# Optimization experiments

Measured on AMD Instinct MI355X. Metric: run time of the kernel, lower is better.

The kernel has to match this reference:

```python
import jax, jax.numpy as jnp
import numpy as np

N_NODES = 50000
N_EDGES = 1600000
D = 128        # fea_dim == hidden_units == dim_z
L = 3          # num_layers


def _gin_params(key, scale=0.05):
    ks = jax.random.split(key, 7)
    return dict(
        W1=jax.random.normal(ks[0], (L, D, D), jnp.float32) * scale,
        b1=jnp.zeros((L, D), jnp.float32),
        W2=jax.random.normal(ks[1], (L, D, D), jnp.float32) * scale,
        b2=jnp.zeros((L, D), jnp.float32),
        eps=jnp.zeros((L,), jnp.float32),
        Wout=jax.random.normal(ks[2], (D, D), jnp.float32) * scale,
        bout=jnp.zeros((D,), jnp.float32),
    )


def setup_inputs() -> dict:
    key = jax.random.key(0)
    k_x, k_s, k_d, k_m, k_sd = jax.random.split(key, 5)
    inp = {
        'x': jax.random.normal(k_x, (N_NODES, D), jnp.float32),
        'edge_src': jax.random.randint(k_s, (N_EDGES,), 0, N_NODES, jnp.int32),
        'edge_dst': jax.random.randint(k_d, (N_EDGES,), 0, N_NODES, jnp.int32),
    }
    for pref, k in (('mean_', k_m), ('std_', k_sd)):
        for name, v in _gin_params(k).items():
            inp[pref + name] = v
    inp['ln_gamma'] = jnp.ones((D,), jnp.float32)
    inp['ln_beta'] = jnp.zeros((D,), jnp.float32)
    return inp


def _gin(x, src, dst, W1, b1, W2, b2, eps, Wout, bout):
    # Standard GIN: h = MLP((1+eps)*h + sum_{j->i} h_j), Sigmoid activation
    h = x
    n = x.shape[0]
    for l in range(L):
        agg = jax.ops.segment_sum(h[src], dst, num_segments=n)  # [N, D]
        h = (1.0 + eps[l]) * h + agg
        h = jax.nn.sigmoid(h @ W1[l] + b1[l]) @ W2[l] + b2[l]
    return h @ Wout + bout  # [N, dim_z]


def _layernorm(v, g, b, eps=1e-5):
    m = jnp.mean(v, axis=-1, keepdims=True)
    var = jnp.var(v, axis=-1, keepdims=True)
    return (v - m) * jax.lax.rsqrt(var + eps) * g + b


def reference(x, edge_src, edge_dst,
              mean_W1, mean_b1, mean_W2, mean_b2, mean_eps, mean_Wout, mean_bout,
              std_W1, std_b1, std_W2, std_b2, std_eps, std_Wout, std_bout,
              ln_gamma, ln_beta):
    mean_v = _layernorm(_gin(x, edge_src, edge_dst, mean_W1, mean_b1, mean_W2,
                             mean_b2, mean_eps, mean_Wout, mean_bout),
                        ln_gamma, ln_beta)
    # NOTE: source applies bn_mean to the std path too (faithful to bug)
    std_v = _layernorm(_gin(x, edge_src, edge_dst, std_W1, std_b1, std_W2,
                            std_b2, std_eps, std_Wout, std_bout),
                       ln_gamma, ln_beta)
    epsilon = jax.random.normal(jax.random.key(42), mean_v.shape, mean_v.dtype)
    samples = mean_v + epsilon * std_v
    return (samples, mean_v, std_v)
```

## Files before the change

kernel.cpp:

```cpp
#include <hip/hip_runtime.h>
#include <math.h>

#define NNODES 50000
#define NEDGES 1600000
#define DIM    128
#define NHID   (NNODES * DIM)
#define TPB    256
#define NTILES ((NNODES + 63) / 64)

#define NBINS  196
#define BINSZ  256
#define EPT    16
#define CHUNK  (TPB * EPT)
#define NCHUNKS ((NEDGES + CHUNK - 1) / CHUNK)
#define BINCAP 10240

typedef unsigned short bf16_t;
typedef __attribute__((ext_vector_type(8))) short short8;
typedef __attribute__((ext_vector_type(4))) float f32x4;

__device__ __forceinline__ float bf_lo(unsigned u) { return __uint_as_float(u << 16); }
__device__ __forceinline__ float bf_hi(unsigned u) { return __uint_as_float(u & 0xFFFF0000u); }
__device__ __forceinline__ bf16_t f2bf(float f) {
    unsigned u = __float_as_uint(f);
    u += 0x7FFFu + ((u >> 16) & 1u);
    return (bf16_t)(u >> 16);
}
__device__ __forceinline__ unsigned pack2bf(float a, float b) {
    return (unsigned)f2bf(a) | ((unsigned)f2bf(b) << 16);
}

union S8U { short8 v; uint4 u4; unsigned us[4]; };

__global__ __launch_bounds__(TPB) void bin_hist_kernel(
    const int* __restrict__ dst, int* __restrict__ gcnt)
{
    __shared__ int lcnt[NBINS];
    const int tid = threadIdx.x;
    for (int i = tid; i < NBINS; i += TPB) lcnt[i] = 0;
    __syncthreads();
    const int base = blockIdx.x * CHUNK;
    #pragma unroll
    for (int k = 0; k < EPT; ++k) {
        int e = base + k * TPB + tid;
        if (e < NEDGES) atomicAdd(&lcnt[dst[e] >> 8], 1);
    }
    __syncthreads();
    for (int i = tid; i < NBINS; i += TPB) {
        int c = lcnt[i];
        if (c) atomicAdd(&gcnt[i], c);
    }
}

__global__ __launch_bounds__(64) void bin_scan_kernel(
    const int* __restrict__ gcnt, int* __restrict__ start, int* __restrict__ bcur,
    int* __restrict__ off)
{
    const int lane = threadIdx.x;
    int c[4];
    int s = 0;
    #pragma unroll
    for (int k = 0; k < 4; ++k) {
        int b = 4 * lane + k;
        c[k] = (b < NBINS) ? gcnt[b] : 0;
        s += c[k];
    }
    int incl = s;
    #pragma unroll
    for (int d = 1; d < 64; d <<= 1) {
        int t = __shfl_up(incl, d);
        if (lane >= d) incl += t;
    }
    int excl = incl - s;
    #pragma unroll
    for (int k = 0; k < 4; ++k) {
        int b = 4 * lane + k;
        if (b < NBINS) { start[b] = excl; bcur[b] = excl; }
        excl += c[k];
    }
    if (lane == 63) { start[NBINS] = excl; off[NNODES] = excl; }
}

__global__ __launch_bounds__(TPB) void bin_scatter_kernel(
    const int* __restrict__ src, const int* __restrict__ dst,
    int* __restrict__ bcur, unsigned* __restrict__ bucket)
{
    __shared__ int lcnt[NBINS];
    __shared__ int lcur[NBINS];
    const int tid = threadIdx.x;
    for (int i = tid; i < NBINS; i += TPB) lcnt[i] = 0;
    __syncthreads();

    unsigned pk[EPT];
    int bn[EPT];
    const int base = blockIdx.x * CHUNK;
    #pragma unroll
    for (int k = 0; k < EPT; ++k) {
        int e = base + k * TPB + tid;
        int b = -1; unsigned p = 0;
        if (e < NEDGES) {
            int d = dst[e];
            int s = src[e];
            b = d >> 8;
            p = ((unsigned)(d & 255) << 16) | (unsigned)s;
            atomicAdd(&lcnt[b], 1);
        }
        pk[k] = p; bn[k] = b;
    }
    __syncthreads();
    for (int i = tid; i < NBINS; i += TPB) {
        int c = lcnt[i];
        lcur[i] = (c > 0) ? atomicAdd(&bcur[i], c) : 0;
    }
    __syncthreads();
    #pragma unroll
    for (int k = 0; k < EPT; ++k) {
        if (bn[k] >= 0) {
            int p = atomicAdd(&lcur[bn[k]], 1);
            bucket[p] = pk[k];
        }
    }
}

__global__ __launch_bounds__(TPB) void build_csr_kernel(
    const int* __restrict__ start, unsigned* __restrict__ bucket,
    int* __restrict__ off)
{
    __shared__ unsigned se[BINCAP];
    __shared__ int lcnt[BINSZ];
    __shared__ int lofs[BINSZ];
    __shared__ int wsum[4];
    const int tid = threadIdx.x;
    const int b = blockIdx.x;
    const int j0 = start[b], j1 = start[b + 1];
    const int n = j1 - j0;

    lcnt[tid] = 0;
    for (int i = tid; i < n; i += TPB) se[i] = bucket[j0 + i];
    __syncthreads();
    for (int i = tid; i < n; i += TPB) atomicAdd(&lcnt[se[i] >> 16], 1);
    __syncthreads();

    const int lane = tid & 63, wid = tid >> 6;
    int v = lcnt[tid];
    int s = v;
    #pragma unroll
    for (int d = 1; d < 64; d <<= 1) {
        int t = __shfl_up(s, d);
        if (lane >= d) s += t;
    }
    if (lane == 63) wsum[wid] = s;
    __syncthreads();
    if (tid == 0) {
        int a = 0;
        #pragma unroll
        for (int k = 0; k < 4; ++k) { int t = wsum[k]; wsum[k] = a; a += t; }
    }
    __syncthreads();
    int excl = wsum[wid] + s - v;
    lofs[tid] = excl;
    int node = b * BINSZ + tid;
    if (node < NNODES) off[node] = j0 + excl;
    __syncthreads();

    for (int i = tid; i < n; i += TPB) {
        unsigned e = se[i];
        int pos = atomicAdd(&lofs[e >> 16], 1);
        bucket[j0 + pos] = e & 0xFFFFu;
    }
}

__global__ __launch_bounds__(TPB) void gather_agg_f32_kernel(
    const float* __restrict__ h, const int* __restrict__ off,
    const unsigned* __restrict__ bucket, float* __restrict__ agg)
{
    int node = blockIdx.x * (TPB / 64) + (threadIdx.x >> 6);
    int lane = threadIdx.x & 63;
    if (node >= NNODES) return;
    int j0 = off[node], j1 = off[node + 1];
    const float* base = h + 2 * lane;
    float ax = 0.0f, ay = 0.0f;
    int j = j0;
    for (; j + 8 <= j1; j += 8) {
        unsigned s[8];
        #pragma unroll
        for (int k = 0; k < 8; ++k) s[k] = bucket[j + k];
        float2 v[8];
        #pragma unroll
        for (int k = 0; k < 8; ++k) v[k] = *(const float2*)(base + (size_t)s[k] * DIM);
        #pragma unroll
        for (int k = 0; k < 8; ++k) { ax += v[k].x; ay += v[k].y; }
    }
    for (; j < j1; ++j) {
        float2 v0 = *(const float2*)(base + (size_t)bucket[j] * DIM);
        ax += v0.x; ay += v0.y;
    }
    *(float2*)(agg + (size_t)node * DIM + 2 * lane) = make_float2(ax, ay);
}

__global__ __launch_bounds__(TPB) void gather_agg_bf16_kernel(
    const bf16_t* __restrict__ hb, const int* __restrict__ off,
    const unsigned* __restrict__ bucket, float* __restrict__ agg)
{
    int node = blockIdx.x * (TPB / 64) + (threadIdx.x >> 6);
    int lane = threadIdx.x & 63;
    if (node >= NNODES) return;
    int j0 = off[node], j1 = off[node + 1];
    const unsigned* base = (const unsigned*)hb + lane;
    float ax = 0.0f, ay = 0.0f;
    int j = j0;
    for (; j + 8 <= j1; j += 8) {
        unsigned s[8];
        #pragma unroll
        for (int k = 0; k < 8; ++k) s[k] = bucket[j + k];
        unsigned u[8];
        #pragma unroll
        for (int k = 0; k < 8; ++k) u[k] = base[(size_t)s[k] * (DIM / 2)];
        #pragma unroll
        for (int k = 0; k < 8; ++k) { ax += bf_lo(u[k]); ay += bf_hi(u[k]); }
    }
    for (; j < j1; ++j) {
        unsigned u0 = base[(size_t)bucket[j] * (DIM / 2)];
        ax += bf_lo(u0); ay += bf_hi(u0);
    }
    *(float2*)(agg + (size_t)node * DIM + 2 * lane) = make_float2(ax, ay);
}

template <class HinT, class HoutT, int MODE, bool HAS_AGG, bool SPLIT>
__global__ __launch_bounds__(TPB) void mfma_gemm_kernel(
    const HinT* __restrict__ hin, const float* __restrict__ agg,
    const float* __restrict__ eps_ptr, int eps_idx,
    const float* __restrict__ W, const float* __restrict__ bias,
    const float* __restrict__ gamma, const float* __restrict__ beta,
    HoutT* __restrict__ out)
{
    __shared__ short sWt[128 * 136];

    const int tid = threadIdx.x;
    #pragma unroll
    for (int it = 0; it < 8; ++it) {
        int idx = it * 256 + tid;
        int n = idx & 127, koct = idx >> 7;
        float f[8];
        #pragma unroll
        for (int j = 0; j < 8; ++j) f[j] = W[(8 * koct + j) * 128 + n];
        uint4 u;
        u.x = pack2bf(f[0], f[1]); u.y = pack2bf(f[2], f[3]);
        u.z = pack2bf(f[4], f[5]); u.w = pack2bf(f[6], f[7]);
        *(uint4*)&sWt[n * 136 + 8 * koct] = u;
    }
    __syncthreads();

    const int lane = tid & 63, w = tid >> 6;
    const int m = lane & 15, quad = lane >> 4;

    short8 bf[32];
    #pragma unroll
    for (int c = 0; c < 8; ++c)
        #pragma unroll
        for (int k0 = 0; k0 < 4; ++k0)
            bf[c * 4 + k0] = *(const short8*)&sWt[(16 * c + m) * 136 + 32 * k0 + 8 * quad];

    const float scale = HAS_AGG ? (1.0f + eps_ptr[eps_idx]) : 1.0f;

    float bias_v[8];
    #pragma unroll
    for (int c = 0; c < 8; ++c) bias_v[c] = bias[16 * c + m];
    float g_v[8], bt_v[8];
    if (MODE == 2) {
        #pragma unroll
        for (int c = 0; c < 8; ++c) { g_v[c] = gamma[16 * c + m]; bt_v[c] = beta[16 * c + m]; }
    }

    for (int t = blockIdx.x; t < NTILES; t += gridDim.x) {
        const int arow = min(t * 64 + 16 * w + m, NNODES - 1);
        const size_t rbase = (size_t)arow * DIM;

        short8 afh[4], afl[4];
        #pragma unroll
        for (int k0 = 0; k0 < 4; ++k0) {
            const int kb = 32 * k0 + 8 * quad;
            if (!HAS_AGG && sizeof(HinT) == 2) {
                afh[k0] = *(const short8*)((const bf16_t*)hin + rbase + kb);
            } else {
                float zf[8];
                if constexpr (sizeof(HinT) == 4) {
                    float4 h0 = *(const float4*)((const float*)hin + rbase + kb);
                    float4 h1 = *(const float4*)((const float*)hin + rbase + kb + 4);
                    zf[0] = h0.x; zf[1] = h0.y; zf[2] = h0.z; zf[3] = h0.w;
                    zf[4] = h1.x; zf[5] = h1.y; zf[6] = h1.z; zf[7] = h1.w;
                } else {
                    uint4 hu = *(const uint4*)((const bf16_t*)hin + rbase + kb);
                    zf[0] = bf_lo(hu.x); zf[1] = bf_hi(hu.x);
                    zf[2] = bf_lo(hu.y); zf[3] = bf_hi(hu.y);
                    zf[4] = bf_lo(hu.z); zf[5] = bf_hi(hu.z);
                    zf[6] = bf_lo(hu.w); zf[7] = bf_hi(hu.w);
                }
                if (HAS_AGG) {
                    float4 a0 = *(const float4*)(agg + rbase + kb);
                    float4 a1 = *(const float4*)(agg + rbase + kb + 4);
                    zf[0] = fmaf(scale, zf[0], a0.x); zf[1] = fmaf(scale, zf[1], a0.y);
                    zf[2] = fmaf(scale, zf[2], a0.z); zf[3] = fmaf(scale, zf[3], a0.w);
                    zf[4] = fmaf(scale, zf[4], a1.x); zf[5] = fmaf(scale, zf[5], a1.y);
                    zf[6] = fmaf(scale, zf[6], a1.z); zf[7] = fmaf(scale, zf[7], a1.w);
                }
                S8U hi;
                hi.us[0] = pack2bf(zf[0], zf[1]); hi.us[1] = pack2bf(zf[2], zf[3]);
                hi.us[2] = pack2bf(zf[4], zf[5]); hi.us[3] = pack2bf(zf[6], zf[7]);
                afh[k0] = hi.v;
                if (SPLIT) {
                    S8U lo;
                    float lw[8];
                    lw[0] = zf[0] - bf_lo(hi.us[0]); lw[1] = zf[1] - bf_hi(hi.us[0]);
                    lw[2] = zf[2] - bf_lo(hi.us[1]); lw[3] = zf[3] - bf_hi(hi.us[1]);
                    lw[4] = zf[4] - bf_lo(hi.us[2]); lw[5] = zf[5] - bf_hi(hi.us[2]);
                    lw[6] = zf[6] - bf_lo(hi.us[3]); lw[7] = zf[7] - bf_hi(hi.us[3]);
                    lo.us[0] = pack2bf(lw[0], lw[1]); lo.us[1] = pack2bf(lw[2], lw[3]);
                    lo.us[2] = pack2bf(lw[4], lw[5]); lo.us[3] = pack2bf(lw[6], lw[7]);
                    afl[k0] = lo.v;
                }
            }
        }

        f32x4 acc[8];
        #pragma unroll
        for (int c = 0; c < 8; ++c) acc[c] = (f32x4){0.f, 0.f, 0.f, 0.f};
        #pragma unroll
        for (int k0 = 0; k0 < 4; ++k0) {
            if (SPLIT) {
                #pragma unroll
                for (int c = 0; c < 8; ++c)
                    acc[c] = __builtin_amdgcn_mfma_f32_16x16x32_bf16(
                        afl[k0], bf[c * 4 + k0], acc[c], 0, 0, 0);
            }
            #pragma unroll
            for (int c = 0; c < 8; ++c)
                acc[c] = __builtin_amdgcn_mfma_f32_16x16x32_bf16(
                    afh[k0], bf[c * 4 + k0], acc[c], 0, 0, 0);
        }

        const int row0 = t * 64 + 16 * w + 4 * quad;
        #pragma unroll
        for (int r = 0; r < 4; ++r) {
            const int grow = row0 + r;
            const bool ok = grow < NNODES;
            float y[8];
            #pragma unroll
            for (int c = 0; c < 8; ++c) y[c] = acc[c][r] + bias_v[c];
            if (MODE == 1) {
                #pragma unroll
                for (int c = 0; c < 8; ++c) y[c] = 1.0f / (1.0f + expf(-y[c]));
            } else if (MODE == 2) {
                float s1 = 0.f, s2 = 0.f;
                #pragma unroll
                for (int c = 0; c < 8; ++c) { s1 += y[c]; s2 = fmaf(y[c], y[c], s2); }
                #pragma unroll
                for (int d = 1; d < 16; d <<= 1) {
                    s1 += __shfl_xor(s1, d);
                    s2 += __shfl_xor(s2, d);
                }
                float mean = s1 * (1.0f / DIM);
                float var  = s2 * (1.0f / DIM) - mean * mean;
                float rstd = rsqrtf(var + 1e-5f);
                #pragma unroll
                for (int c = 0; c < 8; ++c)
                    y[c] = fmaf((y[c] - mean) * rstd, g_v[c], bt_v[c]);
            }
            if (ok) {
                if constexpr (sizeof(HoutT) == 4) {
                    float* op = (float*)out + (size_t)grow * DIM + m;
                    #pragma unroll
                    for (int c = 0; c < 8; ++c) op[16 * c] = y[c];
                } else {
                    bf16_t* op = (bf16_t*)out + (size_t)grow * DIM + m;
                    #pragma unroll
                    for (int c = 0; c < 8; ++c) op[16 * c] = f2bf(y[c]);
                }
            }
        }
    }
}

__device__ __forceinline__ unsigned rotl32(unsigned x, int r) {
    return (x << r) | (x >> (32 - r));
}

__device__ __forceinline__ unsigned threefry_xor(unsigned c0, unsigned c1) {
    const unsigned k0 = 0u, k1 = 42u;
    const unsigned k2 = k0 ^ k1 ^ 0x1BD11BDAu;
    unsigned x0 = c0 + k0;
    unsigned x1 = c1 + k1;
#define TF_ROUND(R) { x0 += x1; x1 = rotl32(x1, R); x1 ^= x0; }
    TF_ROUND(13) TF_ROUND(15) TF_ROUND(26) TF_ROUND(6)
    x0 += k1; x1 += k2 + 1u;
    TF_ROUND(17) TF_ROUND(29) TF_ROUND(16) TF_ROUND(24)
    x0 += k2; x1 += k0 + 2u;
    TF_ROUND(13) TF_ROUND(15) TF_ROUND(26) TF_ROUND(6)
    x0 += k0; x1 += k1 + 3u;
    TF_ROUND(17) TF_ROUND(29) TF_ROUND(16) TF_ROUND(24)
    x0 += k1; x1 += k2 + 4u;
    TF_ROUND(13) TF_ROUND(15) TF_ROUND(26) TF_ROUND(6)
    x0 += k2; x1 += k0 + 5u;
#undef TF_ROUND
    return x0 ^ x1;
}

__device__ __forceinline__ float bits_to_normal(unsigned bits) {
    float f = __uint_as_float((bits >> 9) | 0x3F800000u) - 1.0f;
    const float lo = -0.99999994f;
    float u = __fadd_rn(__fmul_rn(f, 2.0f), lo);
    u = fmaxf(lo, u);
    float w = -log1pf(-(u * u));
    float p;
    if (w < 5.0f) {
        w -= 2.5f;
        p = 2.81022636e-08f;
        p = fmaf(p, w, 3.43273939e-07f);
        p = fmaf(p, w, -3.5233877e-06f);
        p = fmaf(p, w, -4.39150654e-06f);
        p = fmaf(p, w, 0.00021858087f);
        p = fmaf(p, w, -0.00125372503f);
        p = fmaf(p, w, -0.00417768164f);
        p = fmaf(p, w, 0.246640727f);
        p = fmaf(p, w, 1.50140941f);
    } else {
        w = sqrtf(w) - 3.0f;
        p = -0.000200214257f;
        p = fmaf(p, w, 0.000100950558f);
        p = fmaf(p, w, 0.00134934322f);
        p = fmaf(p, w, -0.00367342844f);
        p = fmaf(p, w, 0.00573950773f);
        p = fmaf(p, w, -0.0076224613f);
        p = fmaf(p, w, 0.00943887047f);
        p = fmaf(p, w, 1.00167406f);
        p = fmaf(p, w, 2.83297682f);
    }
    return 1.41421356f * (p * u);
}

__global__ __launch_bounds__(TPB) void samples_kernel(
    const float* __restrict__ mean_v, const float* __restrict__ std_v,
    float* __restrict__ samples)
{
    int t = blockIdx.x * TPB + threadIdx.x;
    if (t >= NHID / 4) return;
    float4 m = ((const float4*)mean_v)[t];
    float4 s = ((const float4*)std_v)[t];
    float e[4];
    #pragma unroll
    for (int q = 0; q < 4; q++) {
        unsigned i = 4u * (unsigned)t + (unsigned)q;
        e[q] = bits_to_normal(threefry_xor(0u, i));
    }
    float4 r;
    r.x = fmaf(e[0], s.x, m.x);
    r.y = fmaf(e[1], s.y, m.y);
    r.z = fmaf(e[2], s.z, m.z);
    r.w = fmaf(e[3], s.w, m.w);
    ((float4*)samples)[t] = r;
}

extern "C" void kernel_launch(void* const* d_in, const int* in_sizes, int n_in,
                              void* d_out, int out_size, void* d_ws, size_t ws_size,
                              hipStream_t stream)
{
    const float* x     = (const float*)d_in[0];
    const int*   esrc  = (const int*)d_in[1];
    const int*   edst  = (const int*)d_in[2];
    const float* prm[2][7];
    for (int p = 0; p < 2; p++)
        for (int i = 0; i < 7; i++)
            prm[p][i] = (const float*)d_in[3 + p * 7 + i];
    const float* gamma = (const float*)d_in[17];
    const float* beta  = (const float*)d_in[18];

    float*  S  = (float*)d_out;
    bf16_t* Sb = (bf16_t*)d_out;
    float*  M  = S + NHID;
    float*  V  = M + NHID;

    int* gcnt  = (int*)d_ws;
    int* start = gcnt + NBINS;
    int* bcur  = start + NBINS + 1;
    int* off   = bcur + NBINS;
    unsigned* bucket = (unsigned*)(off + NNODES + 1);

    const dim3 gChunk(NCHUNKS);
    const dim3 gBin(NBINS);
    const dim3 gGather((NNODES + (TPB / 64) - 1) / (TPB / 64));
    const dim3 gGemm(512);
    const dim3 gSamp((NHID / 4 + TPB - 1) / TPB);

    hipMemsetAsync(gcnt, 0, NBINS * sizeof(int), stream);
    bin_hist_kernel<<<gChunk, TPB, 0, stream>>>(edst, gcnt);
    bin_scan_kernel<<<1, 64, 0, stream>>>(gcnt, start, bcur, off);
    bin_scatter_kernel<<<gChunk, TPB, 0, stream>>>(esrc, edst, bcur, bucket);
    build_csr_kernel<<<gBin, TPB, 0, stream>>>(start, bucket, off);

    gather_agg_f32_kernel<<<gGather, TPB, 0, stream>>>(x, off, bucket, V);

    for (int p = 0; p < 2; p++) {
        const float* W1  = prm[p][0];
        const float* b1  = prm[p][1];
        const float* W2  = prm[p][2];
        const float* b2  = prm[p][3];
        const float* eps = prm[p][4];
        const float* Wo  = prm[p][5];
        const float* bo  = prm[p][6];
        float* AGG = (p == 0) ? M : V;
        float* OUT = (p == 0) ? M : V;

        mfma_gemm_kernel<float, bf16_t, 1, true, true><<<gGemm, TPB, 0, stream>>>(
            x, V, eps, 0, W1, b1, nullptr, nullptr, Sb);
        mfma_gemm_kernel<bf16_t, bf16_t, 0, false, false><<<gGemm, TPB, 0, stream>>>(
            Sb, nullptr, nullptr, 0, W2, b2, nullptr, nullptr, Sb);

        for (int l = 1; l < 3; l++) {
            gather_agg_bf16_kernel<<<gGather, TPB, 0, stream>>>(Sb, off, bucket, AGG);
            mfma_gemm_kernel<bf16_t, bf16_t, 1, true, true><<<gGemm, TPB, 0, stream>>>(
                Sb, AGG, eps, l, W1 + (size_t)l * DIM * DIM, b1 + l * DIM,
                nullptr, nullptr, Sb);
            mfma_gemm_kernel<bf16_t, bf16_t, 0, false, false><<<gGemm, TPB, 0, stream>>>(
                Sb, nullptr, nullptr, 0, W2 + (size_t)l * DIM * DIM, b2 + l * DIM,
                nullptr, nullptr, Sb);
        }

        mfma_gemm_kernel<bf16_t, float, 2, false, false><<<gGemm, TPB, 0, stream>>>(
            Sb, nullptr, nullptr, 0, Wo, bo, gamma, beta, OUT);
    }

    samples_kernel<<<gSamp, TPB, 0, stream>>>(M, V, S);
}
```

Before: 708.9 us.

## Fuse both MLP GEMMs of each GIN layer into one tiled kernel

Adds a kernel that computes the first GEMM (with the split-precision hi/lo bf16 A operand), applies sigmoid, keeps the 64x128 intermediate in LDS, then runs the second GEMM and writes bf16 output. Each GIN layer now needs one launch instead of two. This removes the global-memory round trip of the hidden activation and one launch per layer. In exchange every 64-row tile block stages both weight matrices into LDS, using about 69KB of LDS per block. Because the grid switches from 512 blocks to one block per tile, weight staging is repeated across more blocks, and the output-GEMM launch uses the tile grid as well.

```diff
diff --git a/kernel.cpp b/kernel.cpp
--- a/kernel.cpp
+++ b/kernel.cpp
@@ -224,6 +224,156 @@
         ax += bf_lo(u0); ay += bf_hi(u0);
     }
     *(float2*)(agg + (size_t)node * DIM + 2 * lane) = make_float2(ax, ay);
+}
+
+template <class HinT>
+__global__ __launch_bounds__(TPB, 2) void fused_layer_kernel(
+    const HinT* __restrict__ hin, const float* __restrict__ agg,
+    const float* __restrict__ eps_ptr, int eps_idx,
+    const float* __restrict__ W1, const float* __restrict__ b1,
+    const float* __restrict__ W2, const float* __restrict__ b2,
+    bf16_t* __restrict__ out)
+{
+    __shared__ short sW1t[128 * 136];
+    __shared__ short sW2t[128 * 136];
+    float* y1buf = (float*)sW1t;
+
+    const int tid = threadIdx.x;
+    #pragma unroll
+    for (int it = 0; it < 8; ++it) {
+        int idx = it * 256 + tid;
+        int n = idx & 127, koct = idx >> 7;
+        float f1[8], f2[8];
+        #pragma unroll
+        for (int j = 0; j < 8; ++j) {
+            f1[j] = W1[(8 * koct + j) * 128 + n];
+            f2[j] = W2[(8 * koct + j) * 128 + n];
+        }
+        uint4 u1, u2;
+        u1.x = pack2bf(f1[0], f1[1]); u1.y = pack2bf(f1[2], f1[3]);
+        u1.z = pack2bf(f1[4], f1[5]); u1.w = pack2bf(f1[6], f1[7]);
+        u2.x = pack2bf(f2[0], f2[1]); u2.y = pack2bf(f2[2], f2[3]);
+        u2.z = pack2bf(f2[4], f2[5]); u2.w = pack2bf(f2[6], f2[7]);
+        *(uint4*)&sW1t[n * 136 + 8 * koct] = u1;
+        *(uint4*)&sW2t[n * 136 + 8 * koct] = u2;
+    }
+    __syncthreads();
+
+    const int lane = tid & 63, w = tid >> 6;
+    const int m = lane & 15, quad = lane >> 4;
+
+    short8 bf1[32];
+    #pragma unroll
+    for (int c = 0; c < 8; ++c)
+        #pragma unroll
+        for (int k0 = 0; k0 < 4; ++k0)
+            bf1[c * 4 + k0] = *(const short8*)&sW1t[(16 * c + m) * 136 + 32 * k0 + 8 * quad];
+    __syncthreads();
+
+    const float scale = 1.0f + eps_ptr[eps_idx];
+    float b1v[8], b2v[8];
+    #pragma unroll
+    for (int c = 0; c < 8; ++c) { b1v[c] = b1[16 * c + m]; b2v[c] = b2[16 * c + m]; }
+
+    const int t = blockIdx.x;
+    const int arow = min(t * 64 + 16 * w + m, NNODES - 1);
+    const size_t rbase = (size_t)arow * DIM;
+
+    short8 afh[4], afl[4];
+    #pragma unroll
+    for (int k0 = 0; k0 < 4; ++k0) {
+        const int kb = 32 * k0 + 8 * quad;
+        float zf[8];
+        if constexpr (sizeof(HinT) == 4) {
+            float4 h0 = *(const float4*)((const float*)hin + rbase + kb);
+            float4 h1 = *(const float4*)((const float*)hin + rbase + kb + 4);
+            zf[0] = h0.x; zf[1] = h0.y; zf[2] = h0.z; zf[3] = h0.w;
+            zf[4] = h1.x; zf[5] = h1.y; zf[6] = h1.z; zf[7] = h1.w;
+        } else {
+            uint4 hu = *(const uint4*)((const bf16_t*)hin + rbase + kb);
+            zf[0] = bf_lo(hu.x); zf[1] = bf_hi(hu.x);
+            zf[2] = bf_lo(hu.y); zf[3] = bf_hi(hu.y);
+            zf[4] = bf_lo(hu.z); zf[5] = bf_hi(hu.z);
+            zf[6] = bf_lo(hu.w); zf[7] = bf_hi(hu.w);
+        }
+        float4 a0 = *(const float4*)(agg + rbase + kb);
+        float4 a1 = *(const float4*)(agg + rbase + kb + 4);
+        zf[0] = fmaf(scale, zf[0], a0.x); zf[1] = fmaf(scale, zf[1], a0.y);
+        zf[2] = fmaf(scale, zf[2], a0.z); zf[3] = fmaf(scale, zf[3], a0.w);
+        zf[4] = fmaf(scale, zf[4], a1.x); zf[5] = fmaf(scale, zf[5], a1.y);
+        zf[6] = fmaf(scale, zf[6], a1.z); zf[7] = fmaf(scale, zf[7], a1.w);
+        S8U hi;
+        hi.us[0] = pack2bf(zf[0], zf[1]); hi.us[1] = pack2bf(zf[2], zf[3]);
+        hi.us[2] = pack2bf(zf[4], zf[5]); hi.us[3] = pack2bf(zf[6], zf[7]);
+        afh[k0] = hi.v;
+        S8U lo;
+        float lw[8];
+        lw[0] = zf[0] - bf_lo(hi.us[0]); lw[1] = zf[1] - bf_hi(hi.us[0]);
+        lw[2] = zf[2] - bf_lo(hi.us[1]); lw[3] = zf[3] - bf_hi(hi.us[1]);
+        lw[4] = zf[4] - bf_lo(hi.us[2]); lw[5] = zf[5] - bf_hi(hi.us[2]);
+        lw[6] = zf[6] - bf_lo(hi.us[3]); lw[7] = zf[7] - bf_hi(hi.us[3]);
+        lo.us[0] = pack2bf(lw[0], lw[1]); lo.us[1] = pack2bf(lw[2], lw[3]);
+        lo.us[2] = pack2bf(lw[4], lw[5]); lo.us[3] = pack2bf(lw[6], lw[7]);
+        afl[k0] = lo.v;
+    }
+
+    f32x4 acc[8];
+    #pragma unroll
+    for (int c = 0; c < 8; ++c) acc[c] = (f32x4){0.f, 0.f, 0.f, 0.f};
+    #pragma unroll
+    for (int k0 = 0; k0 < 4; ++k0) {
+        #pragma unroll
+        for (int c = 0; c < 8; ++c)
+            acc[c] = __builtin_amdgcn_mfma_f32_16x16x32_bf16(
+                afl[k0], bf1[c * 4 + k0], acc[c], 0, 0, 0);
+        #pragma unroll
+        for (int c = 0; c < 8; ++c)
+            acc[c] = __builtin_amdgcn_mfma_f32_16x16x32_bf16(
+                afh[k0], bf1[c * 4 + k0], acc[c], 0, 0, 0);
+    }
+
+    const int rloc0 = 16 * w + 4 * quad;
+    #pragma unroll
+    for (int r = 0; r < 4; ++r) {
+        #pragma unroll
+        for (int c = 0; c < 8; ++c) {
+            float y = acc[c][r] + b1v[c];
+            y = 1.0f / (1.0f + expf(-y));
+            y1buf[(rloc0 + r) * 132 + 16 * c + m] = y;
+        }
+    }
+    __syncthreads();
+
+    f32x4 acc2[8];
+    #pragma unroll
+    for (int c = 0; c < 8; ++c) acc2[c] = (f32x4){0.f, 0.f, 0.f, 0.f};
+    #pragma unroll
+    for (int k0 = 0; k0 < 4; ++k0) {
+        const int kb = 32 * k0 + 8 * quad;
+        const float* yp = &y1buf[(16 * w + m) * 132 + kb];
+        float4 p0 = *(const float4*)yp;
+        float4 p1 = *(const float4*)(yp + 4);
+        S8U a2;
+        a2.us[0] = pack2bf(p0.x, p0.y); a2.us[1] = pack2bf(p0.z, p0.w);
+        a2.us[2] = pack2bf(p1.x, p1.y); a2.us[3] = pack2bf(p1.z, p1.w);
+        #pragma unroll
+        for (int c = 0; c < 8; ++c) {
+            short8 b2f = *(const short8*)&sW2t[(16 * c + m) * 136 + kb];
+            acc2[c] = __builtin_amdgcn_mfma_f32_16x16x32_bf16(
+                a2.v, b2f, acc2[c], 0, 0, 0);
+        }
+    }
+
+    const int row0 = t * 64 + 16 * w + 4 * quad;
+    #pragma unroll
+    for (int r = 0; r < 4; ++r) {
+        const int grow = row0 + r;
+        if (grow < NNODES) {
+            bf16_t* op = out + (size_t)grow * DIM + m;
+            #pragma unroll
+            for (int c = 0; c < 8; ++c) op[16 * c] = f2bf(acc2[c][r] + b2v[c]);
+        }
+    }
 }
 
 template <class HinT, class HoutT, int MODE, bool HAS_AGG, bool SPLIT>
@@ -488,7 +638,7 @@
     const dim3 gChunk(NCHUNKS);
     const dim3 gBin(NBINS);
     const dim3 gGather((NNODES + (TPB / 64) - 1) / (TPB / 64));
-    const dim3 gGemm(512);
+    const dim3 gTile(NTILES);
     const dim3 gSamp((NHID / 4 + TPB - 1) / TPB);
 
     hipMemsetAsync(gcnt, 0, NBINS * sizeof(int), stream);
@@ -510,22 +660,17 @@
         float* AGG = (p == 0) ? M : V;
         float* OUT = (p == 0) ? M : V;
 
-        mfma_gemm_kernel<float, bf16_t, 1, true, true><<<gGemm, TPB, 0, stream>>>(
-            x, V, eps, 0, W1, b1, nullptr, nullptr, Sb);
-        mfma_gemm_kernel<bf16_t, bf16_t, 0, false, false><<<gGemm, TPB, 0, stream>>>(
-            Sb, nullptr, nullptr, 0, W2, b2, nullptr, nullptr, Sb);
+        fused_layer_kernel<float><<<gTile, TPB, 0, stream>>>(
+            x, V, eps, 0, W1, b1, W2, b2, Sb);
 
         for (int l = 1; l < 3; l++) {
             gather_agg_bf16_kernel<<<gGather, TPB, 0, stream>>>(Sb, off, bucket, AGG);
-            mfma_gemm_kernel<bf16_t, bf16_t, 1, true, true><<<gGemm, TPB, 0, stream>>>(
+            fused_layer_kernel<bf16_t><<<gTile, TPB, 0, stream>>>(
                 Sb, AGG, eps, l, W1 + (size_t)l * DIM * DIM, b1 + l * DIM,
-                nullptr, nullptr, Sb);
-            mfma_gemm_kernel<bf16_t, bf16_t, 0, false, false><<<gGemm, TPB, 0, stream>>>(
-                Sb, nullptr, nullptr, 0, W2 + (size_t)l * DIM * DIM, b2 + l * DIM,
-                nullptr, nullptr, Sb);
-        }
-
-        mfma_gemm_kernel<bf16_t, float, 2, false, false><<<gGemm, TPB, 0, stream>>>(
+                W2 + (size_t)l * DIM * DIM, b2 + l * DIM, Sb);
+        }
+
+        mfma_gemm_kernel<bf16_t, float, 2, false, false><<<gTile, TPB, 0, stream>>>(
             Sb, nullptr, nullptr, 0, Wo, bo, gamma, beta, OUT);
     }
 
```

Result: no change. 713.7 us (+0.7%).
